# Performance work log

Hardware: AMD Instinct MI355X
Metric: run time of the kernel (lower is better)

The kernel has to match this reference:

```python
import jax, jax.numpy as jnp
import numpy as np
import math

LEVEL_DIMS = [256, 512, 1024, 2048]
B, P, K, D = 8192, 64, 8, 512
EPS = 1e-5  # torch LayerNorm default eps


def _layernorm(x, g, b):
    m = jnp.mean(x, axis=-1, keepdims=True)
    v = jnp.var(x, axis=-1, keepdims=True)
    return (x - m) / jnp.sqrt(v + EPS) * g + b


def _l2norm(x):
    # F.normalize(dim=-1): x / max(||x||_2, 1e-12)
    n = jnp.sqrt(jnp.sum(x * x, axis=-1, keepdims=True))
    return x / jnp.maximum(n, 1e-12)


def setup_inputs() -> dict:
    key = jax.random.key(0)
    ks = iter(jax.random.split(key, 32))
    inp = {}
    for i, dim in enumerate(LEVEL_DIMS):
        inp[f'pooled_{i}'] = jax.random.normal(next(ks), (B, dim), jnp.float32)
        inp[f'proto_{i}'] = jax.random.normal(next(ks), (P, dim), jnp.float32)
        inp[f'ln_g_{i}'] = jnp.ones((2 * dim,), jnp.float32)
        inp[f'ln_b_{i}'] = jnp.zeros((2 * dim,), jnp.float32)
        inp[f'W_{i}'] = jax.random.normal(next(ks), (2 * dim, D), jnp.float32) * (1.0 / math.sqrt(2 * dim))
        inp[f'b_{i}'] = jnp.zeros((D,), jnp.float32)
    inp['text_base'] = jax.random.normal(next(ks), (K, D), jnp.float32)
    inp['logit_scale'] = jnp.ones((1,), jnp.float32)
    return inp


def reference(pooled_0, pooled_1, pooled_2, pooled_3,
              proto_0, proto_1, proto_2, proto_3,
              ln_g_0, ln_g_1, ln_g_2, ln_g_3,
              ln_b_0, ln_b_1, ln_b_2, ln_b_3,
              W_0, W_1, W_2, W_3,
              b_0, b_1, b_2, b_3,
              text_base, logit_scale):
    pooled = [pooled_0, pooled_1, pooled_2, pooled_3]
    proto = [proto_0, proto_1, proto_2, proto_3]
    ln_g = [ln_g_0, ln_g_1, ln_g_2, ln_g_3]
    ln_b = [ln_b_0, ln_b_1, ln_b_2, ln_b_3]
    Ws = [W_0, W_1, W_2, W_3]
    bs = [b_0, b_1, b_2, b_3]

    # text encoder: CLIP embeddings normalized, text_proj=Identity, normalized again (idempotent)
    text_features = _l2norm(text_base)  # [K, D]

    ctxs = []
    for pl, pr, g, bb, W, b in zip(pooled, proto, ln_g, ln_b, Ws, bs):
        proto_ctx = jnp.broadcast_to(jnp.mean(pr, axis=0, keepdims=True), pl.shape)  # [B, C]
        fused = jnp.concatenate([pl, proto_ctx], axis=1)  # [B, 2C]
        h = jax.nn.relu(_layernorm(fused, g, bb) @ W + b)  # [B, D]
        ctxs.append(_l2norm(h))
    image_contexts = jnp.stack(ctxs, axis=1)  # [B, L, D]

    logits = jnp.einsum('kd,bld->bkl', text_features, image_contexts)
    logits = logits / math.sqrt(D)
    logits = logits * jnp.clip(logit_scale, 1e-4, None)
    return jax.nn.softmax(logits, axis=-1)  # [B, K, L]
```

## Files before the change

### kernel.cpp

```cpp
#include <hip/hip_runtime.h>
#include <stdint.h>

typedef __bf16 bf16x8 __attribute__((ext_vector_type(8)));
typedef float f32x4 __attribute__((ext_vector_type(4)));

#define OFF_ABF   0u
#define OFF_GWT   62914560u
#define OFF_H     66846720u
#define OFF_STAT  100401152u
#define OFF_TEXT  100663296u
#define OFF_U     100679680u
#define OFF_GG    100687872u
#define OFF_BB    100696064u
#define OFF_SCAL  100704256u
#define OFF_PMEAN 100704512u
#define WS_TOTAL  100719872u

__host__ __device__ __forceinline__ size_t abf_off(int l) {
  return (size_t)4194304u * (size_t)((1u << l) - 1u);
}
__host__ __device__ __forceinline__ size_t gwt_off(int l) {
  return (size_t)262144u * (size_t)((1u << l) - 1u);
}
__device__ __forceinline__ int pm_off(int l) { return 256 * ((1 << l) - 1); }

__device__ __forceinline__ unsigned short f2bf(float x) {
  return (unsigned short)((__float_as_uint(x) + 0x8000u) >> 16);
}
__device__ __forceinline__ unsigned pack2(float a, float b) {
  return ((__float_as_uint(a) + 0x8000u) >> 16) |
         ((__float_as_uint(b) + 0x8000u) & 0xffff0000u);
}
__device__ __forceinline__ void async_load16(const void* g, void* l) {
  __builtin_amdgcn_global_load_lds((const __attribute__((address_space(1))) void*)g,
                                   (__attribute__((address_space(3))) void*)l,
                                   16, 0, 0);
}

struct PrepArgs {
  const float* pooled[4];
  const float* proto[4];
  const float* W[4];
  const float* g[4];
  const float* beta[4];
  const float* bias[4];
  const float* text;
  const float* lsc;
  char* ws;
};

template <int N4, int R>
__device__ __forceinline__ void aconvG(const float* Pl, char* Ab, float* st,
                                       int C, int rowBase, int lane) {
  float4 v[R][N4];
  const float4* P0 = (const float4*)(Pl + (size_t)rowBase * C);
#pragma unroll
  for (int r = 0; r < R; ++r)
#pragma unroll
    for (int i = 0; i < N4; ++i)
      v[r][i] = P0[(size_t)r * (C >> 2) + lane + 64 * i];
#pragma unroll
  for (int r = 0; r < R; ++r) {
    uint2* D = (uint2*)(Ab + (size_t)(rowBase + r) * C * 2);
    float s1 = 0.f, s2 = 0.f;
#pragma unroll
    for (int i = 0; i < N4; ++i) {
      float4 x = v[r][i];
      s1 += x.x + x.y + x.z + x.w;
      s2 = fmaf(x.x, x.x, s2); s2 = fmaf(x.y, x.y, s2);
      s2 = fmaf(x.z, x.z, s2); s2 = fmaf(x.w, x.w, s2);
      uint2 o;
      o.x = pack2(x.x, x.y);
      o.y = pack2(x.z, x.w);
      D[lane + 64 * i] = o;
    }
#pragma unroll
    for (int off = 1; off < 64; off <<= 1) {
      s1 += __shfl_xor(s1, off);
      s2 += __shfl_xor(s2, off);
    }
    if (lane == 0) {
      st[(size_t)(rowBase + r) * 2] = s1;
      st[(size_t)(rowBase + r) * 2 + 1] = s2;
    }
  }
}

__global__ __launch_bounds__(256, 4) void aconv(PrepArgs A) {
  __shared__ float redP[4][64];
  int t = threadIdx.x, bid = blockIdx.x;
  int w = t >> 6, lane = t & 63;

  if (bid < 1920) {
    int g = bid * 4 + w;
    int l, rowBase;
    if (g < 4096)      { l = 3; rowBase = g * 2; }
    else if (g < 6144) { l = 2; rowBase = (g - 4096) * 4; }
    else if (g < 7168) { l = 1; rowBase = (g - 6144) * 8; }
    else               { l = 0; rowBase = (g - 7168) * 16; }
    int C = 256 << l;
    const float* Pl = A.pooled[l];
    char* Ab = A.ws + OFF_ABF + abf_off(l);
    float* st = (float*)(A.ws + OFF_STAT) + (size_t)l * 8192 * 2;
    if (l == 3)      aconvG<8, 2>(Pl, Ab, st, C, rowBase, lane);
    else if (l == 2) aconvG<4, 4>(Pl, Ab, st, C, rowBase, lane);
    else if (l == 1) aconvG<2, 8>(Pl, Ab, st, C, rowBase, lane);
    else             aconvG<1, 16>(Pl, Ab, st, C, rowBase, lane);
    return;
  }
  float* scal = (float*)(A.ws + OFF_SCAL);
  if (bid < 1980) {
    int p = bid - 1920;
    int l, chunk;
    if (p < 32)      { l = 3; chunk = p; }
    else if (p < 48) { l = 2; chunk = p - 32; }
    else if (p < 56) { l = 1; chunk = p - 48; }
    else             { l = 0; chunk = p - 56; }
    int C = 256 << l;
    int c = chunk * 64 + lane;
    const float* pr = A.proto[l];
    float s = 0.f;
#pragma unroll
    for (int r = 0; r < 16; ++r) s += pr[(size_t)(w * 16 + r) * C + c];
    redP[w][lane] = s;
    __syncthreads();
    if (t < 64) {
      float pmv = (redP[0][t] + redP[1][t] + redP[2][t] + redP[3][t]) * (1.0f / 64.0f);
      ((float*)(A.ws + OFF_PMEAN))[pm_off(l) + chunk * 64 + t] = pmv;
      float s1 = pmv, s2 = pmv * pmv;
#pragma unroll
      for (int off = 1; off < 64; off <<= 1) {
        s1 += __shfl_xor(s1, off);
        s2 += __shfl_xor(s2, off);
      }
      if (t == 0) {
        atomicAdd(&scal[l], s1);
        atomicAdd(&scal[4 + l], s2);
      }
    }
    return;
  }
  float* r1 = &redP[0][0];
  float* tf = (float*)(A.ws + OFF_TEXT);
  for (int r = 0; r < 8; ++r) {
    float p = 0.f;
    for (int c = t; c < 512; c += 256) {
      float v = A.text[r * 512 + c];
      p += v * v;
    }
    r1[t] = p;
    __syncthreads();
    for (int o = 128; o > 0; o >>= 1) {
      if (t < o) r1[t] += r1[t + o];
      __syncthreads();
    }
    float inv = 1.0f / fmaxf(sqrtf(r1[0]), 1e-12f);
    __syncthreads();
    for (int c = t; c < 512; c += 256) tf[r * 512 + c] = A.text[r * 512 + c] * inv;
  }
  if (t == 0) {
    float s = fmaxf(A.lsc[0], 1e-4f);
    scal[8] = s * 0.04419417382415922f;
  }
}

__global__ __launch_bounds__(256) void wtrans(PrepArgs A) {
  __shared__ unsigned short tile[128][66];
  __shared__ float redG[4][128], redB[4][128], redU[4][128];
  __shared__ float gsh[64], bsh[64], psh[64];
  int t = threadIdx.x, bid = blockIdx.x;
  int l, idl;
  if (bid < 256)      { l = 3; idl = bid; }
  else if (bid < 384) { l = 2; idl = bid - 256; }
  else if (bid < 448) { l = 1; idl = bid - 384; }
  else                { l = 0; idl = bid - 448; }
  int C = 256 << l;
  int sid = idl >> 2, dchunk = idl & 3;
  int j0 = sid * 64, d0 = dchunk * 128;
  bool top = (j0 < C);

  if (t < 64) {
    float gv = A.g[l][j0 + t];
    gsh[t] = gv;
    bsh[t] = A.beta[l][j0 + t];
    if (!top)
      psh[t] = ((const float*)(A.ws + OFF_PMEAN))[pm_off(l) + (j0 - C) + t] * gv;
  }
  __syncthreads();

  int w = t >> 6, L = t & 63;
  const float* W = A.W[l];
  float2 v[16];
#pragma unroll
  for (int r = 0; r < 16; ++r) {
    int j = j0 + w * 16 + r;
    v[r] = *(const float2*)(W + (size_t)j * 512 + d0 + 2 * L);
  }
  float gp0 = 0.f, gp1 = 0.f, bp0 = 0.f, bp1 = 0.f, up0 = 0.f, up1 = 0.f;
#pragma unroll
  for (int r = 0; r < 16; ++r) {
    int jl = w * 16 + r;
    float g = gsh[jl], b = bsh[jl];
    gp0 = fmaf(g, v[r].x, gp0); gp1 = fmaf(g, v[r].y, gp1);
    bp0 = fmaf(b, v[r].x, bp0); bp1 = fmaf(b, v[r].y, bp1);
    if (top) {
      tile[2 * L][jl] = f2bf(g * v[r].x);
      tile[2 * L + 1][jl] = f2bf(g * v[r].y);
    } else {
      float p = psh[jl];
      up0 = fmaf(p, v[r].x, up0); up1 = fmaf(p, v[r].y, up1);
    }
  }
  redG[w][2 * L] = gp0; redG[w][2 * L + 1] = gp1;
  redB[w][2 * L] = bp0; redB[w][2 * L + 1] = bp1;
  if (!top) { redU[w][2 * L] = up0; redU[w][2 * L + 1] = up1; }
  __syncthreads();

  if (t < 128) {
    int d = l * 512 + d0 + t;
    float G = redG[0][t] + redG[1][t] + redG[2][t] + redG[3][t];
    float B = redB[0][t] + redB[1][t] + redB[2][t] + redB[3][t];
    atomicAdd(&((float*)(A.ws + OFF_GG))[d], G);
    atomicAdd(&((float*)(A.ws + OFF_BB))[d], B);
    if (!top) {
      float U = redU[0][t] + redU[1][t] + redU[2][t] + redU[3][t];
      atomicAdd(&((float*)(A.ws + OFF_U))[d], U);
    }
  }
  if (top) {
    unsigned short* gwT = (unsigned short*)(A.ws + OFF_GWT + gwt_off(l));
    int d = t >> 1, jh = (t & 1) * 32;
    const unsigned* trow = (const unsigned*)&tile[d][jh];
    uint4 a = make_uint4(trow[0], trow[1], trow[2], trow[3]);
    uint4 b = make_uint4(trow[4], trow[5], trow[6], trow[7]);
    uint4* dst = (uint4*)(gwT + (size_t)(d0 + d) * C + j0 + jh);
    dst[0] = a; dst[1] = b;
  }
}

struct G2Args {
  char* ws;
  const float* bias[4];
};

__global__ __launch_bounds__(256, 3) void gemm2(G2Args A) {
  __shared__ __align__(16) char lds[18944];
  char* ws = A.ws;
  int t = threadIdx.x, bid = blockIdx.x;
  int l = 3 - (bid >> 8);
  int rb = (bid >> 2) & 63, cb = bid & 3;
  int C = 256 << l;
  int m0 = rb * 128, n0 = cb * 128;

  float* uArr  = (float*)(lds + 16384);
  float* gArr  = (float*)(lds + 16896);
  float* bArr  = (float*)(lds + 17408);
  float* rowM  = (float*)(lds + 17920);
  float* rowIS = (float*)(lds + 18432);
  const float* scal = (const float*)(ws + OFF_SCAL);

  if (t < 128) {
    int idx = l * 512 + n0 + t;
    uArr[t] = ((const float*)(ws + OFF_U))[idx];
    gArr[t] = ((const float*)(ws + OFF_GG))[idx];
    bArr[t] = ((const float*)(ws + OFF_BB))[idx] + A.bias[l][n0 + t];
  } else {
    int r = t - 128;
    const float* st = (const float*)(ws + OFF_STAT) + (size_t)(l * 8192 + m0 + r) * 2;
    float s1 = st[0], s2 = st[1];
    float inv2C = 1.0f / (float)(2 * C);
    float mr = (s1 + scal[l]) * inv2C;
    float var = (s2 + scal[4 + l]) * inv2C - mr * mr;
    rowM[r] = mr;
    rowIS[r] = rsqrtf(var + 1e-5f);
  }

  int w = t >> 6, lane = t & 63, quad = lane >> 4, lc = lane & 15;
  const char* Abf = ws + OFF_ABF + abf_off(l);
  const char* Bw  = ws + OFF_GWT + gwt_off(l);
  const char* aP[2]; const char* bP[2];
  char* aD[2]; char* bD[2];
#pragma unroll
  for (int i = 0; i < 2; ++i) {
    int li = i * 256 + t;
    int rr = li >> 2, kq = li & 3;
    aP[i] = Abf + ((size_t)(m0 + rr) * C + kq * 8) * 2;
    bP[i] = Bw  + ((size_t)(n0 + rr) * C + kq * 8) * 2;
    aD[i] = lds + i * 4096 + w * 1024;
    bD[i] = lds + 8192 + i * 4096 + w * 1024;
  }
  int wr = (w >> 1) * 64, wc = (w & 1) * 64;
  const char* aF = lds + (wr + lc) * 64 + quad * 16;
  const char* bF = lds + 8192 + (wc + lc) * 64 + quad * 16;

  f32x4 acc[4][4] = {};
  for (int k0 = 0; k0 < C; k0 += 32) {
    async_load16(aP[0], aD[0]); async_load16(aP[1], aD[1]);
    async_load16(bP[0], bD[0]); async_load16(bP[1], bD[1]);
    aP[0] += 64; aP[1] += 64; bP[0] += 64; bP[1] += 64;
    __syncthreads();
    bf16x8 av[4];
#pragma unroll
    for (int rt = 0; rt < 4; ++rt) av[rt] = *(const bf16x8*)(aF + rt * 1024);
#pragma unroll
    for (int ct = 0; ct < 4; ++ct) {
      bf16x8 bv = *(const bf16x8*)(bF + ct * 1024);
#pragma unroll
      for (int rt = 0; rt < 4; ++rt)
        acc[rt][ct] = __builtin_amdgcn_mfma_f32_16x16x32_bf16(av[rt], bv, acc[rt][ct], 0, 0, 0);
    }
    __syncthreads();
  }

  char* Hl = ws + OFF_H + (size_t)l * 8388608;
#pragma unroll
  for (int rt = 0; rt < 4; ++rt) {
#pragma unroll
    for (int ct = 0; ct < 4; ++ct) {
      int nl = wc + ct * 16 + lc;
      float uu = uArr[nl], gg = gArr[nl], bb = bArr[nl];
      f32x4 a = acc[rt][ct];
#pragma unroll
      for (int reg = 0; reg < 4; ++reg) {
        int ml = wr + rt * 16 + quad * 4 + reg;
        float h = fmaf(a[reg] + uu - rowM[ml] * gg, rowIS[ml], bb);
        h = fmaxf(h, 0.f);
        float hp = __shfl_xor(h, 1);
        if (!(lc & 1)) {
          unsigned pkv = pack2(h, hp);
          *(unsigned*)(Hl + ((size_t)(m0 + ml) * 512 + n0 + nl) * 2) = pkv;
        }
      }
    }
  }
}

__global__ __launch_bounds__(256) void postK(const char* ws, float* out) {
  __shared__ float textL[4096];
  int t = threadIdx.x, b = blockIdx.x;
  const float* tf = (const float*)(ws + OFF_TEXT);
  for (int i = t; i < 4096; i += 256) textL[i] = tf[i];
  __syncthreads();
  float scale = ((const float*)(ws + OFF_SCAL))[8];
  int row = b * 16 + (t >> 4), q = t & 15;
  float lg[4][8];
#pragma unroll
  for (int l = 0; l < 4; ++l) {
    const uint4* hp = (const uint4*)(ws + OFF_H + (size_t)l * 8388608 +
                                     ((size_t)row * 512 + q * 32) * 2);
    float np = 0.f;
    float dp[8] = {};
#pragma unroll
    for (int ch = 0; ch < 4; ++ch) {
      uint4 u = hp[ch];
      int d0 = q * 32 + ch * 8;
      unsigned uw[4] = {u.x, u.y, u.z, u.w};
#pragma unroll
      for (int p = 0; p < 4; ++p) {
        float v0 = __uint_as_float(uw[p] << 16);
        float v1 = __uint_as_float(uw[p] & 0xffff0000u);
        int dd = d0 + p * 2;
        np = fmaf(v0, v0, np);
        np = fmaf(v1, v1, np);
#pragma unroll
        for (int k = 0; k < 8; ++k) {
          dp[k] = fmaf(v0, textL[k * 512 + dd], dp[k]);
          dp[k] = fmaf(v1, textL[k * 512 + dd + 1], dp[k]);
        }
      }
    }
#pragma unroll
    for (int off = 1; off < 16; off <<= 1) {
      np += __shfl_xor(np, off);
#pragma unroll
      for (int k = 0; k < 8; ++k) dp[k] += __shfl_xor(dp[k], off);
    }
    float innorm = scale / fmaxf(sqrtf(np), 1e-12f);
#pragma unroll
    for (int k = 0; k < 8; ++k) lg[l][k] = dp[k] * innorm;
  }
  if (q == 0) {
    float4* op = (float4*)out + (size_t)row * 8;
#pragma unroll
    for (int k = 0; k < 8; ++k) {
      float a = lg[0][k], b2 = lg[1][k], c = lg[2][k], d = lg[3][k];
      float mx = fmaxf(fmaxf(a, b2), fmaxf(c, d));
      float e0 = __expf(a - mx), e1 = __expf(b2 - mx);
      float e2 = __expf(c - mx), e3 = __expf(d - mx);
      float inv = 1.0f / (e0 + e1 + e2 + e3);
      op[k] = make_float4(e0 * inv, e1 * inv, e2 * inv, e3 * inv);
    }
  }
}

extern "C" void kernel_launch(void* const* d_in, const int* in_sizes, int n_in,
                              void* d_out, int out_size, void* d_ws, size_t ws_size,
                              hipStream_t stream) {
  (void)n_in; (void)out_size;
  if (ws_size < (size_t)WS_TOTAL) return;
  char* ws = (char*)d_ws;
  bool dict = (in_sizes[1] == 64 * 256);
  PrepArgs pa;
  for (int l = 0; l < 4; ++l) {
    if (dict) {
      pa.pooled[l] = (const float*)d_in[6 * l + 0];
      pa.proto[l]  = (const float*)d_in[6 * l + 1];
      pa.g[l]      = (const float*)d_in[6 * l + 2];
      pa.beta[l]   = (const float*)d_in[6 * l + 3];
      pa.W[l]      = (const float*)d_in[6 * l + 4];
      pa.bias[l]   = (const float*)d_in[6 * l + 5];
    } else {
      pa.pooled[l] = (const float*)d_in[l];
      pa.proto[l]  = (const float*)d_in[4 + l];
      pa.g[l]      = (const float*)d_in[8 + l];
      pa.beta[l]   = (const float*)d_in[12 + l];
      pa.W[l]      = (const float*)d_in[16 + l];
      pa.bias[l]   = (const float*)d_in[20 + l];
    }
  }
  pa.text = (const float*)d_in[24];
  pa.lsc = (const float*)d_in[25];
  pa.ws = ws;

  hipMemsetAsync(ws + OFF_U, 0, 3 * 8192 + 256, stream);
  aconv<<<1981, 256, 0, stream>>>(pa);
  wtrans<<<480, 256, 0, stream>>>(pa);

  G2Args g2;
  g2.ws = ws;
  for (int l = 0; l < 4; ++l) g2.bias[l] = pa.bias[l];
  gemm2<<<1024, 256, 0, stream>>>(g2);
  postK<<<512, 256, 0, stream>>>(ws, (float*)d_out);
}
```

Measured before the change: 297.8 us.

## Fuse activation bf16 conversion and row stats into GEMM; drop aconv kernel

Removes the separate aconv pre-pass, which converted pooled activations to bf16 and wrote per-row sums. The GEMM now loads fp32 activations directly, packs them to bf16 into swizzled LDS, and accumulates row sum and sum-of-squares on the fly to build the LayerNorm statistics in the epilogue. Prototype means move into wtrans, text normalization and scale move into postK, and the wtrans transpose store is widened. This removes a full fp32 read plus bf16 write and re-read of activations, but puts register-staged conversion and ALU work inside the GEMM main loop, which may hurt its overlap of loads with compute.

```diff
diff --git a/kernel.cpp b/kernel.cpp
--- a/kernel.cpp
+++ b/kernel.cpp
@@ -4,25 +4,17 @@
 typedef __bf16 bf16x8 __attribute__((ext_vector_type(8)));
 typedef float f32x4 __attribute__((ext_vector_type(4)));
 
-#define OFF_ABF   0u
 #define OFF_GWT   62914560u
 #define OFF_H     66846720u
-#define OFF_STAT  100401152u
-#define OFF_TEXT  100663296u
 #define OFF_U     100679680u
 #define OFF_GG    100687872u
 #define OFF_BB    100696064u
 #define OFF_SCAL  100704256u
-#define OFF_PMEAN 100704512u
 #define WS_TOTAL  100719872u
 
-__host__ __device__ __forceinline__ size_t abf_off(int l) {
-  return (size_t)4194304u * (size_t)((1u << l) - 1u);
-}
 __host__ __device__ __forceinline__ size_t gwt_off(int l) {
   return (size_t)262144u * (size_t)((1u << l) - 1u);
 }
-__device__ __forceinline__ int pm_off(int l) { return 256 * ((1 << l) - 1); }
 
 __device__ __forceinline__ unsigned short f2bf(float x) {
   return (unsigned short)((__float_as_uint(x) + 0x8000u) >> 16);
@@ -49,125 +41,11 @@
   char* ws;
 };
 
-template <int N4, int R>
-__device__ __forceinline__ void aconvG(const float* Pl, char* Ab, float* st,
-                                       int C, int rowBase, int lane) {
-  float4 v[R][N4];
-  const float4* P0 = (const float4*)(Pl + (size_t)rowBase * C);
-#pragma unroll
-  for (int r = 0; r < R; ++r)
-#pragma unroll
-    for (int i = 0; i < N4; ++i)
-      v[r][i] = P0[(size_t)r * (C >> 2) + lane + 64 * i];
-#pragma unroll
-  for (int r = 0; r < R; ++r) {
-    uint2* D = (uint2*)(Ab + (size_t)(rowBase + r) * C * 2);
-    float s1 = 0.f, s2 = 0.f;
-#pragma unroll
-    for (int i = 0; i < N4; ++i) {
-      float4 x = v[r][i];
-      s1 += x.x + x.y + x.z + x.w;
-      s2 = fmaf(x.x, x.x, s2); s2 = fmaf(x.y, x.y, s2);
-      s2 = fmaf(x.z, x.z, s2); s2 = fmaf(x.w, x.w, s2);
-      uint2 o;
-      o.x = pack2(x.x, x.y);
-      o.y = pack2(x.z, x.w);
-      D[lane + 64 * i] = o;
-    }
-#pragma unroll
-    for (int off = 1; off < 64; off <<= 1) {
-      s1 += __shfl_xor(s1, off);
-      s2 += __shfl_xor(s2, off);
-    }
-    if (lane == 0) {
-      st[(size_t)(rowBase + r) * 2] = s1;
-      st[(size_t)(rowBase + r) * 2 + 1] = s2;
-    }
-  }
-}
-
-__global__ __launch_bounds__(256, 4) void aconv(PrepArgs A) {
-  __shared__ float redP[4][64];
-  int t = threadIdx.x, bid = blockIdx.x;
-  int w = t >> 6, lane = t & 63;
-
-  if (bid < 1920) {
-    int g = bid * 4 + w;
-    int l, rowBase;
-    if (g < 4096)      { l = 3; rowBase = g * 2; }
-    else if (g < 6144) { l = 2; rowBase = (g - 4096) * 4; }
-    else if (g < 7168) { l = 1; rowBase = (g - 6144) * 8; }
-    else               { l = 0; rowBase = (g - 7168) * 16; }
-    int C = 256 << l;
-    const float* Pl = A.pooled[l];
-    char* Ab = A.ws + OFF_ABF + abf_off(l);
-    float* st = (float*)(A.ws + OFF_STAT) + (size_t)l * 8192 * 2;
-    if (l == 3)      aconvG<8, 2>(Pl, Ab, st, C, rowBase, lane);
-    else if (l == 2) aconvG<4, 4>(Pl, Ab, st, C, rowBase, lane);
-    else if (l == 1) aconvG<2, 8>(Pl, Ab, st, C, rowBase, lane);
-    else             aconvG<1, 16>(Pl, Ab, st, C, rowBase, lane);
-    return;
-  }
-  float* scal = (float*)(A.ws + OFF_SCAL);
-  if (bid < 1980) {
-    int p = bid - 1920;
-    int l, chunk;
-    if (p < 32)      { l = 3; chunk = p; }
-    else if (p < 48) { l = 2; chunk = p - 32; }
-    else if (p < 56) { l = 1; chunk = p - 48; }
-    else             { l = 0; chunk = p - 56; }
-    int C = 256 << l;
-    int c = chunk * 64 + lane;
-    const float* pr = A.proto[l];
-    float s = 0.f;
-#pragma unroll
-    for (int r = 0; r < 16; ++r) s += pr[(size_t)(w * 16 + r) * C + c];
-    redP[w][lane] = s;
-    __syncthreads();
-    if (t < 64) {
-      float pmv = (redP[0][t] + redP[1][t] + redP[2][t] + redP[3][t]) * (1.0f / 64.0f);
-      ((float*)(A.ws + OFF_PMEAN))[pm_off(l) + chunk * 64 + t] = pmv;
-      float s1 = pmv, s2 = pmv * pmv;
-#pragma unroll
-      for (int off = 1; off < 64; off <<= 1) {
-        s1 += __shfl_xor(s1, off);
-        s2 += __shfl_xor(s2, off);
-      }
-      if (t == 0) {
-        atomicAdd(&scal[l], s1);
-        atomicAdd(&scal[4 + l], s2);
-      }
-    }
-    return;
-  }
-  float* r1 = &redP[0][0];
-  float* tf = (float*)(A.ws + OFF_TEXT);
-  for (int r = 0; r < 8; ++r) {
-    float p = 0.f;
-    for (int c = t; c < 512; c += 256) {
-      float v = A.text[r * 512 + c];
-      p += v * v;
-    }
-    r1[t] = p;
-    __syncthreads();
-    for (int o = 128; o > 0; o >>= 1) {
-      if (t < o) r1[t] += r1[t + o];
-      __syncthreads();
-    }
-    float inv = 1.0f / fmaxf(sqrtf(r1[0]), 1e-12f);
-    __syncthreads();
-    for (int c = t; c < 512; c += 256) tf[r * 512 + c] = A.text[r * 512 + c] * inv;
-  }
-  if (t == 0) {
-    float s = fmaxf(A.lsc[0], 1e-4f);
-    scal[8] = s * 0.04419417382415922f;
-  }
-}
-
 __global__ __launch_bounds__(256) void wtrans(PrepArgs A) {
   __shared__ unsigned short tile[128][66];
   __shared__ float redG[4][128], redB[4][128], redU[4][128];
   __shared__ float gsh[64], bsh[64], psh[64];
+  __shared__ float redP[4][64];
   int t = threadIdx.x, bid = blockIdx.x;
   int l, idl;
   if (bid < 256)      { l = 3; idl = bid; }
@@ -178,17 +56,42 @@
   int sid = idl >> 2, dchunk = idl & 3;
   int j0 = sid * 64, d0 = dchunk * 128;
   bool top = (j0 < C);
+  int w = t >> 6, L = t & 63;
+  float* scal = (float*)(A.ws + OFF_SCAL);
 
   if (t < 64) {
-    float gv = A.g[l][j0 + t];
-    gsh[t] = gv;
+    gsh[t] = A.g[l][j0 + t];
     bsh[t] = A.beta[l][j0 + t];
-    if (!top)
-      psh[t] = ((const float*)(A.ws + OFF_PMEAN))[pm_off(l) + (j0 - C) + t] * gv;
+  }
+  if (!top) {
+    const float* pr = A.proto[l];
+    int cb0 = j0 - C;
+    float s = 0.f;
+#pragma unroll
+    for (int r = 0; r < 16; ++r) s += pr[(size_t)(w * 16 + r) * C + cb0 + L];
+    redP[w][L] = s;
   }
   __syncthreads();
-
-  int w = t >> 6, L = t & 63;
+  if (!top) {
+    if (t < 64) {
+      float pmv = (redP[0][t] + redP[1][t] + redP[2][t] + redP[3][t]) * (1.0f / 64.0f);
+      psh[t] = pmv * gsh[t];
+      if (dchunk == 0) {
+        float s1 = pmv, s2 = pmv * pmv;
+#pragma unroll
+        for (int off = 1; off < 64; off <<= 1) {
+          s1 += __shfl_xor(s1, off);
+          s2 += __shfl_xor(s2, off);
+        }
+        if (t == 0) {
+          atomicAdd(&scal[l], s1);
+          atomicAdd(&scal[4 + l], s2);
+        }
+      }
+    }
+    __syncthreads();
+  }
+
   const float* W = A.W[l];
   float2 v[16];
 #pragma unroll
@@ -231,15 +134,18 @@
     unsigned short* gwT = (unsigned short*)(A.ws + OFF_GWT + gwt_off(l));
     int d = t >> 1, jh = (t & 1) * 32;
     const unsigned* trow = (const unsigned*)&tile[d][jh];
-    uint4 a = make_uint4(trow[0], trow[1], trow[2], trow[3]);
-    uint4 b = make_uint4(trow[4], trow[5], trow[6], trow[7]);
+    uint4 q0 = make_uint4(trow[0], trow[1], trow[2], trow[3]);
+    uint4 q1 = make_uint4(trow[4], trow[5], trow[6], trow[7]);
+    uint4 q2 = make_uint4(trow[8], trow[9], trow[10], trow[11]);
+    uint4 q3 = make_uint4(trow[12], trow[13], trow[14], trow[15]);
     uint4* dst = (uint4*)(gwT + (size_t)(d0 + d) * C + j0 + jh);
-    dst[0] = a; dst[1] = b;
+    dst[0] = q0; dst[1] = q1; dst[2] = q2; dst[3] = q3;
   }
 }
 
 struct G2Args {
   char* ws;
+  const float* pooled[4];
   const float* bias[4];
 };
 
@@ -264,41 +170,58 @@
     uArr[t] = ((const float*)(ws + OFF_U))[idx];
     gArr[t] = ((const float*)(ws + OFF_GG))[idx];
     bArr[t] = ((const float*)(ws + OFF_BB))[idx] + A.bias[l][n0 + t];
-  } else {
-    int r = t - 128;
-    const float* st = (const float*)(ws + OFF_STAT) + (size_t)(l * 8192 + m0 + r) * 2;
-    float s1 = st[0], s2 = st[1];
-    float inv2C = 1.0f / (float)(2 * C);
-    float mr = (s1 + scal[l]) * inv2C;
-    float var = (s2 + scal[4 + l]) * inv2C - mr * mr;
-    rowM[r] = mr;
-    rowIS[r] = rsqrtf(var + 1e-5f);
   }
 
   int w = t >> 6, lane = t & 63, quad = lane >> 4, lc = lane & 15;
-  const char* Abf = ws + OFF_ABF + abf_off(l);
-  const char* Bw  = ws + OFF_GWT + gwt_off(l);
-  const char* aP[2]; const char* bP[2];
-  char* aD[2]; char* bD[2];
+  const char* Bw = ws + OFF_GWT + gwt_off(l);
+  const char* bP[2]; char* bD[2];
 #pragma unroll
   for (int i = 0; i < 2; ++i) {
     int li = i * 256 + t;
     int rr = li >> 2, kq = li & 3;
-    aP[i] = Abf + ((size_t)(m0 + rr) * C + kq * 8) * 2;
-    bP[i] = Bw  + ((size_t)(n0 + rr) * C + kq * 8) * 2;
-    aD[i] = lds + i * 4096 + w * 1024;
+    bP[i] = Bw + ((size_t)(n0 + rr) * C + kq * 8) * 2;
     bD[i] = lds + 8192 + i * 4096 + w * 1024;
   }
+  int rA = t >> 2, kq = t & 3;
+  const float* aG0 = A.pooled[l] + (size_t)(m0 + rA) * C + kq * 8;
+  const float* aG1 = aG0 + (size_t)64 * C;
+  int gsw = kq ^ ((rA >> 1) & 3);
+  char* aW0 = lds + rA * 64 + gsw * 16;
+  char* aW1 = aW0 + 64 * 64;
   int wr = (w >> 1) * 64, wc = (w & 1) * 64;
-  const char* aF = lds + (wr + lc) * 64 + quad * 16;
+  int ag = quad ^ (((wr + lc) >> 1) & 3);
+  const char* aF = lds + (wr + lc) * 64 + ag * 16;
   const char* bF = lds + 8192 + (wc + lc) * 64 + quad * 16;
 
   f32x4 acc[4][4] = {};
+  float s1a = 0.f, s2a = 0.f, s1b = 0.f, s2b = 0.f;
+  f32x4 a0 = *(const f32x4*)aG0, a1 = *(const f32x4*)(aG0 + 4);
+  f32x4 a2 = *(const f32x4*)aG1, a3 = *(const f32x4*)(aG1 + 4);
   for (int k0 = 0; k0 < C; k0 += 32) {
-    async_load16(aP[0], aD[0]); async_load16(aP[1], aD[1]);
+    if (k0) __syncthreads();
     async_load16(bP[0], bD[0]); async_load16(bP[1], bD[1]);
-    aP[0] += 64; aP[1] += 64; bP[0] += 64; bP[1] += 64;
+    bP[0] += 64; bP[1] += 64;
+    *(uint4*)aW0 = make_uint4(pack2(a0[0], a0[1]), pack2(a0[2], a0[3]),
+                              pack2(a1[0], a1[1]), pack2(a1[2], a1[3]));
+    *(uint4*)aW1 = make_uint4(pack2(a2[0], a2[1]), pack2(a2[2], a2[3]),
+                              pack2(a3[0], a3[1]), pack2(a3[2], a3[3]));
+    s1a += ((a0[0] + a0[1]) + (a0[2] + a0[3])) + ((a1[0] + a1[1]) + (a1[2] + a1[3]));
+    s2a = fmaf(a0[0], a0[0], s2a); s2a = fmaf(a0[1], a0[1], s2a);
+    s2a = fmaf(a0[2], a0[2], s2a); s2a = fmaf(a0[3], a0[3], s2a);
+    s2a = fmaf(a1[0], a1[0], s2a); s2a = fmaf(a1[1], a1[1], s2a);
+    s2a = fmaf(a1[2], a1[2], s2a); s2a = fmaf(a1[3], a1[3], s2a);
+    s1b += ((a2[0] + a2[1]) + (a2[2] + a2[3])) + ((a3[0] + a3[1]) + (a3[2] + a3[3]));
+    s2b = fmaf(a2[0], a2[0], s2b); s2b = fmaf(a2[1], a2[1], s2b);
+    s2b = fmaf(a2[2], a2[2], s2b); s2b = fmaf(a2[3], a2[3], s2b);
+    s2b = fmaf(a3[0], a3[0], s2b); s2b = fmaf(a3[1], a3[1], s2b);
+    s2b = fmaf(a3[2], a3[2], s2b); s2b = fmaf(a3[3], a3[3], s2b);
     __syncthreads();
+    if (k0 + 32 < C) {
+      aG0 += 32; aG1 += 32;
+      a0 = *(const f32x4*)aG0; a1 = *(const f32x4*)(aG0 + 4);
+      a2 = *(const f32x4*)aG1; a3 = *(const f32x4*)(aG1 + 4);
+    }
+    __builtin_amdgcn_sched_barrier(0);
     bf16x8 av[4];
 #pragma unroll
     for (int rt = 0; rt < 4; ++rt) av[rt] = *(const bf16x8*)(aF + rt * 1024);
@@ -309,8 +232,24 @@
       for (int rt = 0; rt < 4; ++rt)
         acc[rt][ct] = __builtin_amdgcn_mfma_f32_16x16x32_bf16(av[rt], bv, acc[rt][ct], 0, 0, 0);
     }
-    __syncthreads();
-  }
+  }
+
+#pragma unroll
+  for (int off = 1; off < 4; off <<= 1) {
+    s1a += __shfl_xor(s1a, off); s2a += __shfl_xor(s2a, off);
+    s1b += __shfl_xor(s1b, off); s2b += __shfl_xor(s2b, off);
+  }
+  if ((t & 3) == 0) {
+    float inv2C = 1.0f / (float)(2 * C);
+    float spro = scal[l], sqpro = scal[4 + l];
+    float mra = (s1a + spro) * inv2C;
+    rowM[rA] = mra;
+    rowIS[rA] = rsqrtf((s2a + sqpro) * inv2C - mra * mra + 1e-5f);
+    float mrb = (s1b + spro) * inv2C;
+    rowM[64 + rA] = mrb;
+    rowIS[64 + rA] = rsqrtf((s2b + sqpro) * inv2C - mrb * mrb + 1e-5f);
+  }
+  __syncthreads();
 
   char* Hl = ws + OFF_H + (size_t)l * 8388608;
 #pragma unroll
@@ -335,13 +274,27 @@
   }
 }
 
-__global__ __launch_bounds__(256) void postK(const char* ws, float* out) {
+__global__ __launch_bounds__(256) void postK(const char* ws, const float* text,
+                                             const float* lsc, float* out) {
   __shared__ float textL[4096];
   int t = threadIdx.x, b = blockIdx.x;
-  const float* tf = (const float*)(ws + OFF_TEXT);
-  for (int i = t; i < 4096; i += 256) textL[i] = tf[i];
+  {
+    int gq = t >> 5, lq = t & 31;
+    float v[16];
+    float pa = 0.f;
+#pragma unroll
+    for (int i = 0; i < 16; ++i) {
+      v[i] = text[gq * 512 + lq + 32 * i];
+      pa = fmaf(v[i], v[i], pa);
+    }
+#pragma unroll
+    for (int off = 1; off < 32; off <<= 1) pa += __shfl_xor(pa, off);
+    float inv = 1.0f / fmaxf(sqrtf(pa), 1e-12f);
+#pragma unroll
+    for (int i = 0; i < 16; ++i) textL[gq * 512 + lq + 32 * i] = v[i] * inv;
+  }
   __syncthreads();
-  float scale = ((const float*)(ws + OFF_SCAL))[8];
+  float scale = fmaxf(lsc[0], 1e-4f) * 0.04419417382415922f;
   int row = b * 16 + (t >> 4), q = t & 15;
   float lg[4][8];
 #pragma unroll
@@ -423,12 +376,14 @@
   pa.ws = ws;
 
   hipMemsetAsync(ws + OFF_U, 0, 3 * 8192 + 256, stream);
-  aconv<<<1981, 256, 0, stream>>>(pa);
   wtrans<<<480, 256, 0, stream>>>(pa);
 
   G2Args g2;
   g2.ws = ws;
-  for (int l = 0; l < 4; ++l) g2.bias[l] = pa.bias[l];
+  for (int l = 0; l < 4; ++l) {
+    g2.pooled[l] = pa.pooled[l];
+    g2.bias[l] = pa.bias[l];
+  }
   gemm2<<<1024, 256, 0, stream>>>(g2);
-  postK<<<512, 256, 0, stream>>>(ws, (float*)d_out);
-}
+  postK<<<512, 256, 0, stream>>>(ws, pa.text, pa.lsc, (float*)d_out);
+}
```

New measurement: 303.6 us. Within noise of the previous version (+2.0%).
